# Performance work log

Measured on AMD Instinct MI355X. Metric: run time of the kernel, lower is better.

The kernel has to match this reference:

```python
import jax, jax.numpy as jnp
import numpy as np

B, H, W, C = 4, 16, 16, 1024
D_INNER, D_STATE, DT_RANK, K = 2048, 32, 64, 4
NTXT = 4096
L = H * W


def _selective_scan(u, dt, A, Bs, Cs, Ds):
    # u, dt: (B,K,D,L); A: (K,D,N); Bs, Cs: (B,K,N,L); Ds: (K,D)
    u_l = jnp.moveaxis(u, -1, 0)
    dt_l = jnp.moveaxis(dt, -1, 0)
    B_l = jnp.moveaxis(Bs, -1, 0)
    C_l = jnp.moveaxis(Cs, -1, 0)
    h0 = jnp.zeros(u.shape[:3] + (A.shape[-1],), u.dtype)

    def step(h, xs):
        u_t, dt_t, B_t, C_t = xs
        dA = jnp.exp(dt_t[..., None] * A)                    # (B,K,D,N)
        h = h * dA + dt_t[..., None] * B_t[:, :, None, :] * u_t[..., None]
        y = jnp.einsum('bkdn,bkn->bkd', h, C_t)
        return h, y

    _, ys = jax.lax.scan(step, h0, (u_l, dt_l, B_l, C_l))
    return jnp.moveaxis(ys, 0, -1) + Ds[None, :, :, None] * u


def _forward(image_embeds, text_embeds, in_proj_w, conv_w, conv_b, x_proj_w,
             dt_proj_w, dt_proj_b, A_logs, Ds, out_norm_w, out_norm_b, out_proj_w):
    b = image_embeds.shape[0]
    # in_proj -> split into x (scanned) and z (gate)
    xz = jnp.einsum('bhwc,ec->bhwe', image_embeds, in_proj_w)    # (B,H,W,2*D_INNER)
    x, z = jnp.split(xz, 2, axis=-1)
    # depthwise conv 3x3 + SiLU
    xc = jnp.transpose(x, (0, 3, 1, 2))                          # (B,D,H,W)
    xc = jax.lax.conv_general_dilated(xc, conv_w, (1, 1), 'SAME',
                                      feature_group_count=D_INNER,
                                      dimension_numbers=('NCHW', 'OIHW', 'NCHW'))
    xc = jax.nn.silu(xc + conv_b[None, :, None, None])
    # cross-scan: row-major, col-major, and their reverses
    xm = xc.reshape(b, D_INNER, L)
    xt = jnp.transpose(xc, (0, 1, 3, 2)).reshape(b, D_INNER, L)
    xs = jnp.stack([xm, xt, xm[..., ::-1], xt[..., ::-1]], axis=1)  # (B,4,D,L)
    # low-rank input-dependent params
    x_dbl = jnp.einsum('bkdl,kcd->bkcl', xs, x_proj_w)
    dts, Bmat, Cmat = jnp.split(x_dbl, [DT_RANK, DT_RANK + D_STATE], axis=2)
    dts = jnp.einsum('bkrl,kdr->bkdl', dts, dt_proj_w)
    dts = jax.nn.softplus(dts + dt_proj_b[None, :, :, None])
    A = -jnp.exp(A_logs).reshape(K, D_INNER, D_STATE)
    ys = _selective_scan(xs, dts, A, Bmat, Cmat, Ds.reshape(K, D_INNER))
    # cross-merge
    y = ys[:, 0] + ys[:, 2, :, ::-1]
    y_col = ys[:, 1] + ys[:, 3, :, ::-1]
    y = y + jnp.transpose(y_col.reshape(b, D_INNER, W, H), (0, 1, 3, 2)).reshape(b, D_INNER, L)
    # out_norm (LayerNorm over channels) + gate + out_proj
    y = jnp.transpose(y, (0, 2, 1))                              # (B,L,D)
    mu = y.mean(-1, keepdims=True)
    var = ((y - mu) ** 2).mean(-1, keepdims=True)
    y = (y - mu) * jax.lax.rsqrt(var + 1e-5) * out_norm_w + out_norm_b
    y = y.reshape(b, H, W, D_INNER) * jax.nn.silu(z)
    enhanced = jnp.einsum('bhwd,cd->bhwc', y, out_proj_w)        # (B,H,W,C)
    # L2 normalize + similarity logits
    img = enhanced / jnp.linalg.norm(enhanced, axis=-1, keepdims=True)
    txt = text_embeds / jnp.linalg.norm(text_embeds, axis=-1, keepdims=True)
    return jnp.matmul(img, txt.T)                                # (B,H,W,NTXT)


def setup_inputs() -> dict:
    key = jax.random.key(0)
    ks = jax.random.split(key, 8)
    s = 0.02
    return dict(
        image_embeds=jax.random.normal(ks[0], (B, H, W, C), jnp.float32),
        text_embeds=jax.random.normal(ks[1], (NTXT, C), jnp.float32),
        in_proj_w=jax.random.normal(ks[2], (2 * D_INNER, C), jnp.float32) * s,
        conv_w=jax.random.normal(ks[3], (D_INNER, 1, 3, 3), jnp.float32) * s,
        conv_b=jnp.zeros((D_INNER,), jnp.float32),
        x_proj_w=jax.random.normal(ks[4], (K, DT_RANK + 2 * D_STATE, D_INNER), jnp.float32) * s,
        dt_proj_w=jax.random.normal(ks[5], (K, D_INNER, DT_RANK), jnp.float32) * s,
        dt_proj_b=jax.random.normal(ks[6], (K, D_INNER), jnp.float32) * s,
        A_logs=jnp.log(jnp.broadcast_to(jnp.arange(1, D_STATE + 1, dtype=jnp.float32), (K * D_INNER, D_STATE)).copy()),
        Ds=jnp.ones((K * D_INNER,), jnp.float32),
        out_norm_w=jnp.ones((D_INNER,), jnp.float32),
        out_norm_b=jnp.zeros((D_INNER,), jnp.float32),
        out_proj_w=jax.random.normal(ks[7], (C, D_INNER), jnp.float32) * s,
    )


def reference(image_embeds, text_embeds, in_proj_w, conv_w, conv_b, x_proj_w,
              dt_proj_w, dt_proj_b, A_logs, Ds, out_norm_w, out_norm_b, out_proj_w):
    return _forward(image_embeds, text_embeds, in_proj_w, conv_w, conv_b, x_proj_w,
                    dt_proj_w, dt_proj_b, A_logs, Ds, out_norm_w, out_norm_b, out_proj_w)
```

## Files before the change

### kernel.cpp

```cpp
#include <hip/hip_runtime.h>
#include <math.h>


typedef unsigned short u16;
typedef __attribute__((ext_vector_type(8))) short short8;
typedef __attribute__((ext_vector_type(8))) unsigned short ushort8;
typedef __attribute__((ext_vector_type(4))) float f32x4;

__device__ __forceinline__ float sigmoidf_(float x) { return 1.f / (1.f + __expf(-x)); }

__device__ __forceinline__ u16 f2bf(float x) {
  unsigned u = __float_as_uint(x);
  unsigned r = u + 0x7FFFu + ((u >> 16) & 1u);
  return (u16)(r >> 16);
}
__device__ __forceinline__ float bf2f(u16 h) { return __uint_as_float((unsigned)h << 16); }

__device__ __forceinline__ void gl_lds16(const u16* g, u16* l) {
  __builtin_amdgcn_global_load_lds((__attribute__((address_space(1))) void*)g,
                                   (__attribute__((address_space(3))) void*)l, 16, 0, 0);
}

__global__ __launch_bounds__(256) void cvt_swz(
    const float* __restrict__ in, u16* __restrict__ hi, u16* __restrict__ lo,
    int R, int bpr , int lda)
{
  long t = (long)blockIdx.x * 256 + threadIdx.x;
  if (t >= (long)R * bpr) return;
  int m = (int)(t / bpr);
  int rb = (int)(t - (long)m * bpr);
  int kc = rb >> 2, g = rb & 3;
  const float* src = in + (long)m * lda + (kc << 5) + (g << 2);
  float4 a = *(const float4*)src;
  float4 b = *(const float4*)(src + 16);
  float v[8] = {a.x, a.y, a.z, a.w, b.x, b.y, b.z, b.w};
  ushort8 H, L;
#pragma unroll
  for (int q = 0; q < 8; q++) {
    u16 h = f2bf(v[q]);
    H[q] = h;
    L[q] = f2bf(v[q] - bf2f(h));
  }
  long off = (((long)kc * R + m) << 5) + ((long)((g ^ ((m >> 1) & 3)) << 3));
  *(ushort8*)(hi + off) = H;
  *(ushort8*)(lo + off) = L;
}

__global__ __launch_bounds__(256) void mfma_nt(
    const u16* __restrict__ Ahi, const u16* __restrict__ Alo,
    const u16* __restrict__ Bhi, const u16* __restrict__ Blo,
    float* __restrict__ C, int Mtot, int Ntot, int Ksteps, int ldc,
    int sArows, int sBrows, int bmod, long sC, long sCk, int ksplit)
{
  __shared__ u16 smem[16384];
  const int tid = threadIdx.x, lane = tid & 63, wid = tid >> 6;
  const int zb = blockIdx.z / ksplit, zk = blockIdx.z - zb * ksplit;
  const int m0 = blockIdx.y << 7, n0 = blockIdx.x << 7;

  const u16* sg;
  long row0;
  int tot;
  if (wid < 2) { row0 = (long)zb * sArows + m0; tot = Mtot; sg = wid ? Alo : Ahi; }
  else         { row0 = (long)(zb % bmod) * sBrows + n0; tot = Ntot; sg = (wid == 3) ? Blo : Bhi; }
  u16* sl = smem + (wid << 12);
  const int laneoff = lane << 3;

  f32x4 acc[4][4];
#pragma unroll
  for (int i = 0; i < 4; i++)
#pragma unroll
    for (int j = 0; j < 4; j++) acc[i][j] = (f32x4)0.f;

  const int wr = wid >> 1, wc = wid & 1;
  const int fr = lane & 15, g = lane >> 4;
  int offA[4], offB[4];
#pragma unroll
  for (int i = 0; i < 4; i++) {
    int rA = wr * 64 + i * 16 + fr;
    offA[i] = rA * 32 + ((g ^ ((rA >> 1) & 3)) << 3);
    int rB = wc * 64 + i * 16 + fr;
    offB[i] = rB * 32 + ((g ^ ((rB >> 1) & 3)) << 3);
  }

  for (int kc = 0; kc < Ksteps; ++kc) {
    const int kcg = zk * Ksteps + kc;
    const u16* s = sg + ((long)kcg * tot + row0) * 32 + laneoff;
#pragma unroll
    for (int c = 0; c < 8; ++c) gl_lds16(s + c * 512, sl + c * 512 + laneoff);
    asm volatile("s_waitcnt vmcnt(0)" ::: "memory");
    __syncthreads();

    short8 ah[4], al[4], bh[4], bl[4];
#pragma unroll
    for (int i = 0; i < 4; i++) {
      ah[i] = *(const short8*)(smem + offA[i]);
      al[i] = *(const short8*)(smem + 4096 + offA[i]);
      bh[i] = *(const short8*)(smem + 8192 + offB[i]);
      bl[i] = *(const short8*)(smem + 12288 + offB[i]);
    }
#pragma unroll
    for (int i = 0; i < 4; i++)
#pragma unroll
      for (int j = 0; j < 4; j++) {
        acc[i][j] = __builtin_amdgcn_mfma_f32_16x16x32_bf16(ah[i], bh[j], acc[i][j], 0, 0, 0);
        acc[i][j] = __builtin_amdgcn_mfma_f32_16x16x32_bf16(ah[i], bl[j], acc[i][j], 0, 0, 0);
        acc[i][j] = __builtin_amdgcn_mfma_f32_16x16x32_bf16(al[i], bh[j], acc[i][j], 0, 0, 0);
      }
    __syncthreads();
  }

  float* Cb = C + (long)zb * sC + (long)zk * sCk;
  const int r0 = m0 + wr * 64, c0 = n0 + wc * 64;
#pragma unroll
  for (int i = 0; i < 4; i++)
#pragma unroll
    for (int j = 0; j < 4; j++) {
      const long cc = c0 + j * 16 + fr;
#pragma unroll
      for (int q = 0; q < 4; q++)
        Cb[(long)(r0 + i * 16 + g * 4 + q) * ldc + cc] = acc[i][j][q];
    }
}

__global__ __launch_bounds__(256) void sum8(float* __restrict__ px)
{
  long t = (long)blockIdx.x * 256 + threadIdx.x;
  if (t >= 524288) return;
  float s = px[t];
#pragma unroll
  for (int p = 1; p < 8; p++) s += px[(long)p * 524288 + t];
  px[t] = s;
}

__global__ __launch_bounds__(256) void zero_buf(float4* __restrict__ p)
{
  p[(long)blockIdx.x * 256 + threadIdx.x] = (float4){0.f, 0.f, 0.f, 0.f};
}

__global__ __launch_bounds__(256) void conv_scatter_bf16(
    const float* __restrict__ xz, const float* __restrict__ cw,
    const float* __restrict__ cb, u16* __restrict__ hi, u16* __restrict__ lo)
{
  const int p = blockIdx.x & 255;
  const int b = blockIdx.x >> 8;
  const int h = p >> 4, w = p & 15;
  const int l1 = (w << 4) + h;
  const int pos[4] = {p, l1, 255 - p, 255 - l1};
#pragma unroll
  for (int it = 0; it < 8; it++) {
    const int d = it * 256 + threadIdx.x;
    float acc = cb[d];
#pragma unroll
    for (int dh = 0; dh < 3; dh++) {
      const int hh = h + dh - 1;
      if (hh < 0 || hh > 15) continue;
#pragma unroll
      for (int dw = 0; dw < 3; dw++) {
        const int ww = w + dw - 1;
        if (ww < 0 || ww > 15) continue;
        acc = fmaf(xz[((long)(b * 256 + (hh << 4) + ww)) * 4096 + d],
                   cw[d * 9 + dh * 3 + dw], acc);
      }
    }
    const float sv = acc * sigmoidf_(acc);
    const u16 hv = f2bf(sv);
    const u16 lv = f2bf(sv - bf2f(hv));
    const int kc = d >> 5, dd = d & 31;
    const int g0 = (dd < 16) ? (dd >> 2) : ((dd - 16) >> 2);
    const int slot = (dd < 16) ? (dd & 3) : 4 + ((dd - 16) & 3);
#pragma unroll
    for (int kk = 0; kk < 4; kk++) {
      const int m = (b * 4 + kk) * 256 + pos[kk];
      const long off = (((long)kc * 4096 + m) << 5) + ((g0 ^ ((m >> 1) & 3)) << 3) + slot;
      hi[off] = hv;
      lo[off] = lv;
    }
  }
}

__global__ __launch_bounds__(256) void scan_fused(
    const u16* __restrict__ xs_hi, const u16* __restrict__ xs_lo,
    const float* __restrict__ xdbl, const float* __restrict__ w_dt,
    const float* __restrict__ b_dt, const float* __restrict__ A_logs,
    const float* __restrict__ Dsv, float* __restrict__ ym)
{
  const int tid = threadIdx.x;
  const int sub = tid & 1;
  const int dl = tid >> 1;
  const int d = blockIdx.x * 128 + dl;
  const int k = blockIdx.y, b = blockIdx.z;
  const int bk = b * 4 + k;
  const int kd = k * 2048 + d;
  const int n0 = sub * 16;

  float a[16], hst[16];
#pragma unroll
  for (int j = 0; j < 16; j++) {
    a[j] = -__expf(A_logs[(long)kd * 32 + n0 + j]);
    hst[j] = 0.f;
  }
  const float Dval = Dsv[kd];
  const float bias = b_dt[kd];

  float wdt[32];
  const float* wp = w_dt + (long)kd * 64 + sub * 32;
#pragma unroll
  for (int j = 0; j < 32; j += 4) *(float4*)&wdt[j] = *(const float4*)(wp + j);

  const int dd = d & 31;
  const int g0 = (dd < 16) ? (dd >> 2) : ((dd - 16) >> 2);
  const int slot = (dd < 16) ? (dd & 3) : 4 + ((dd - 16) & 3);
  const int kcl = dl >> 5;

  const float* xb = xdbl + (long)bk * 256 * 128;
  const int mbase = bk * 256;
  const long obase = (long)b * 256 * 2048 + d;

  __shared__ float xd[32][128];
  __shared__ u16 uh[4][32][32];
  __shared__ u16 ul[4][32][32];

  for (int l0 = 0; l0 < 256; l0 += 32) {
    __syncthreads();
#pragma unroll
    for (int i = 0; i < 4; i++) {
      const int idx = i * 256 + tid;
      const int r = idx >> 5, c = idx & 31;
      *(float4*)&xd[r][c * 4] = *(const float4*)(xb + (l0 + r) * 128 + c * 4);
    }
#pragma unroll
    for (int i = 0; i < 2; i++) {
      const int j = i * 256 + tid;
      const int kc2 = j >> 7, r = (j >> 2) & 31, part = j & 3;
      const long go = (((long)(blockIdx.x * 4 + kc2) * 4096 + mbase + l0 + r) << 5) + part * 8;
      *(ushort8*)&uh[kc2][r][part * 8] = *(const ushort8*)(xs_hi + go);
      *(ushort8*)&ul[kc2][r][part * 8] = *(const ushort8*)(xs_lo + go);
    }
    __syncthreads();

    for (int ls = 0; ls < 32; ls++) {
      const int l = l0 + ls;
      const int m = mbase + l;
      float da = 0.f;
#pragma unroll
      for (int r4 = 0; r4 < 8; r4++) {
        const float4 xv = *(const float4*)&xd[ls][sub * 32 + r4 * 4];
        da = fmaf(wdt[r4 * 4 + 0], xv.x, da);
        da = fmaf(wdt[r4 * 4 + 1], xv.y, da);
        da = fmaf(wdt[r4 * 4 + 2], xv.z, da);
        da = fmaf(wdt[r4 * 4 + 3], xv.w, da);
      }
      da += __shfl_xor(da, 1);
      const float xsp = da + bias;
      const float dt = (xsp > 20.f) ? xsp : log1pf(__expf(xsp));
      const int sw = ((g0 ^ ((m >> 1) & 3)) << 3) + slot;
      const float u = bf2f(uh[kcl][ls][sw]) + bf2f(ul[kcl][ls][sw]);
      const float dtu = dt * u;
      float y = 0.f;
#pragma unroll
      for (int j = 0; j < 16; j++) {
        const float dA = __expf(a[j] * dt);
        hst[j] = fmaf(hst[j], dA, dtu * xd[ls][64 + n0 + j]);
        y = fmaf(hst[j], xd[ls][96 + n0 + j], y);
      }
      y += __shfl_xor(y, 1);
      if (sub == 0) {
        int p;
        if (k == 0) p = l;
        else if (k == 1) p = ((l & 15) << 4) + (l >> 4);
        else if (k == 2) p = 255 - l;
        else { const int lr = 255 - l; p = ((lr & 15) << 4) + (lr >> 4); }
        atomicAdd(&ym[obase + (long)p * 2048], fmaf(Dval, u, y));
      }
    }
  }
}

__global__ __launch_bounds__(256) void ln_gate_cvt(
    const float* __restrict__ ym, const float* __restrict__ xz,
    const float* __restrict__ lw, const float* __restrict__ lb,
    u16* __restrict__ hi, u16* __restrict__ lo)
{
  const int row = blockIdx.x;
  const int tid = threadIdx.x;
  const float* yr = ym + (long)row * 2048;

  __shared__ float sg[2048];
  __shared__ float sm[8];
  float v[8];
  float s = 0.f, ss = 0.f;
#pragma unroll
  for (int i = 0; i < 8; i++) {
    const float t = yr[i * 256 + tid];
    v[i] = t;
    s += t;
    ss += t * t;
  }
#pragma unroll
  for (int off = 32; off > 0; off >>= 1) {
    s += __shfl_down(s, off);
    ss += __shfl_down(ss, off);
  }
  const int lane = tid & 63, wid = tid >> 6;
  if (lane == 0) { sm[wid] = s; sm[4 + wid] = ss; }
  __syncthreads();
  const float S = sm[0] + sm[1] + sm[2] + sm[3];
  const float SS = sm[4] + sm[5] + sm[6] + sm[7];
  const float mu = S * (1.f / 2048.f);
  const float var = SS * (1.f / 2048.f) - mu * mu;
  const float inv = rsqrtf(var + 1e-5f);
#pragma unroll
  for (int i = 0; i < 8; i++) {
    const int d = i * 256 + tid;
    const float yn = (v[i] - mu) * inv * lw[d] + lb[d];
    const float zz = xz[(long)row * 4096 + 2048 + d];
    sg[d] = yn * zz * sigmoidf_(zz);
  }
  __syncthreads();
  const int kc = tid >> 2, g = tid & 3;
  const int c0 = kc * 32 + g * 4;
  ushort8 H, L;
#pragma unroll
  for (int q = 0; q < 4; q++) {
    const float f0 = sg[c0 + q], f1 = sg[c0 + 16 + q];
    const u16 h0 = f2bf(f0), h1 = f2bf(f1);
    H[q] = h0; H[4 + q] = h1;
    L[q] = f2bf(f0 - bf2f(h0));
    L[4 + q] = f2bf(f1 - bf2f(h1));
  }
  const long off = (((long)kc * 1024 + row) << 5) + ((long)((g ^ ((row >> 1) & 3)) << 3));
  *(ushort8*)(hi + off) = H;
  *(ushort8*)(lo + off) = L;
}

template <int P>
__global__ __launch_bounds__(256) void l2cvt(
    const float* __restrict__ in, long pstride,
    u16* __restrict__ hi, u16* __restrict__ lo, int R)
{
  const int row = blockIdx.x;
  const int tid = threadIdx.x;
  __shared__ float sg[1024];
  __shared__ float sm[4];
  float ss = 0.f;
  for (int i = tid; i < 1024; i += 256) {
    float v = in[(long)row * 1024 + i];
#pragma unroll
    for (int p2 = 1; p2 < P; p2++) v += in[(long)p2 * pstride + (long)row * 1024 + i];
    sg[i] = v;
    ss += v * v;
  }
#pragma unroll
  for (int off = 32; off > 0; off >>= 1) ss += __shfl_down(ss, off);
  const int lane = tid & 63, wid = tid >> 6;
  if (lane == 0) sm[wid] = ss;
  __syncthreads();
  const float sc = rsqrtf(sm[0] + sm[1] + sm[2] + sm[3]);
  if (tid < 128) {
    const int kc = tid >> 2, g = tid & 3;
    const int c0 = kc * 32 + g * 4;
    ushort8 H, L;
#pragma unroll
    for (int q = 0; q < 4; q++) {
      const float f0 = sg[c0 + q] * sc, f1 = sg[c0 + 16 + q] * sc;
      const u16 h0 = f2bf(f0), h1 = f2bf(f1);
      H[q] = h0; H[4 + q] = h1;
      L[q] = f2bf(f0 - bf2f(h0));
      L[4 + q] = f2bf(f1 - bf2f(h1));
    }
    const long off = (((long)kc * R + row) << 5) + ((long)((g ^ ((row >> 1) & 3)) << 3));
    *(ushort8*)(hi + off) = H;
    *(ushort8*)(lo + off) = L;
  }
}

extern "C" void kernel_launch(void* const* d_in, const int* in_sizes, int n_in,
                              void* d_out, int out_size, void* d_ws, size_t ws_size,
                              hipStream_t stream)
{
  const float* img = (const float*)d_in[0];
  const float* txt = (const float*)d_in[1];
  const float* w_in = (const float*)d_in[2];
  const float* conv_w = (const float*)d_in[3];
  const float* conv_b = (const float*)d_in[4];
  const float* w_x = (const float*)d_in[5];
  const float* w_dt = (const float*)d_in[6];
  const float* b_dt = (const float*)d_in[7];
  const float* A_logs = (const float*)d_in[8];
  const float* Dsv = (const float*)d_in[9];
  const float* ln_w = (const float*)d_in[10];
  const float* ln_b = (const float*)d_in[11];
  const float* w_out = (const float*)d_in[12];
  float* out = (float*)d_out;

  float* ws = (float*)d_ws;
  float* xz = ws;
  float* Cr = ws + 4194304;
  u16* imgsw_h = (u16*)Cr;
  u16* imgsw_l = (u16*)(Cr + 524288);
  u16* w_insw_h = (u16*)(Cr + 1048576);
  u16* w_insw_l = (u16*)(Cr + 3145728);
  u16* xs_hi = (u16*)Cr;
  u16* xs_lo = (u16*)(Cr + 4194304);
  u16* outgsw_h = (u16*)Cr;
  u16* outgsw_l = (u16*)(Cr + 1048576);
  u16* w_outsw_h = (u16*)(Cr + 2097152);
  u16* w_outsw_l = (u16*)(Cr + 3145728);
  u16* enhsw_h = (u16*)(Cr + 4194304);
  u16* enhsw_l = (u16*)(Cr + 4718592);
  u16* w_xsw_h = (u16*)(ws + 12582912);
  u16* w_xsw_l = (u16*)(ws + 13107200);
  float* ym = ws + 13631488;
  u16* txtnsw_h = (u16*)xz;
  u16* txtnsw_l = (u16*)(xz + 2097152);

  float* ob = (float*)d_out;
  float* px8 = ob;
  float* xdbl = px8;
  float* px4 = ob;

  cvt_swz<<<512, 256, 0, stream>>>(img, imgsw_h, imgsw_l, 1024, 128, 1024);
  cvt_swz<<<2048, 256, 0, stream>>>(w_in, w_insw_h, w_insw_l, 4096, 128, 1024);
  cvt_swz<<<512, 256, 0, stream>>>(w_x, w_xsw_h, w_xsw_l, 512, 256, 2048);

  mfma_nt<<<dim3(32, 8, 1), 256, 0, stream>>>(imgsw_h, imgsw_l, w_insw_h, w_insw_l,
                                              xz, 1024, 4096, 32, 4096, 0, 0, 1, 0, 0, 1);

  conv_scatter_bf16<<<dim3(1024), 256, 0, stream>>>(xz, conv_w, conv_b, xs_hi, xs_lo);

  mfma_nt<<<dim3(1, 2, 128), 256, 0, stream>>>(xs_hi, xs_lo, w_xsw_h, w_xsw_l,
                                               px8, 4096, 512, 8, 128, 256, 128, 4,
                                               32768, 524288, 8);
  sum8<<<2048, 256, 0, stream>>>(px8);
  zero_buf<<<2048, 256, 0, stream>>>((float4*)ym);

  scan_fused<<<dim3(16, 4, 4), 256, 0, stream>>>(xs_hi, xs_lo, xdbl, w_dt, b_dt,
                                                 A_logs, Dsv, ym);

  ln_gate_cvt<<<dim3(1024), 256, 0, stream>>>(ym, xz, ln_w, ln_b, outgsw_h, outgsw_l);

  cvt_swz<<<1024, 256, 0, stream>>>(w_out, w_outsw_h, w_outsw_l, 1024, 256, 2048);

  mfma_nt<<<dim3(8, 8, 4), 256, 0, stream>>>(outgsw_h, outgsw_l, w_outsw_h, w_outsw_l,
                                             px4, 1024, 1024, 16, 1024, 0, 0, 1,
                                             0, 1048576, 4);

  l2cvt<4><<<dim3(1024), 256, 0, stream>>>(px4, 1048576, enhsw_h, enhsw_l, 1024);
  l2cvt<1><<<dim3(4096), 256, 0, stream>>>(txt, 0, txtnsw_h, txtnsw_l, 4096);

  mfma_nt<<<dim3(32, 8, 1), 256, 0, stream>>>(enhsw_h, enhsw_l, txtnsw_h, txtnsw_l,
                                              out, 1024, 4096, 32, 4096, 0, 0, 1, 0, 0, 1);
}
```

Before: 523.7 us.

## Split scan state across 4 lanes and precompute dt per chunk in shared memory

```diff
diff --git a/kernel.cpp b/kernel.cpp
--- a/kernel.cpp
+++ b/kernel.cpp
@@ -185,40 +185,39 @@
     const float* __restrict__ Dsv, float* __restrict__ ym)
 {
   const int tid = threadIdx.x;
-  const int sub = tid & 1;
-  const int dl = tid >> 1;
-  const int d = blockIdx.x * 128 + dl;
   const int k = blockIdx.y, b = blockIdx.z;
   const int bk = b * 4 + k;
+  const int dbase = blockIdx.x << 6;
+  const int mbase = bk * 256;
+  const int kc0 = dbase >> 5;
+
+  const int dc = tid >> 2, sub = tid & 3;
+  const int d = dbase + dc;
   const int kd = k * 2048 + d;
-  const int n0 = sub * 16;
-
-  float a[16], hst[16];
-#pragma unroll
-  for (int j = 0; j < 16; j++) {
+  const int n0 = sub * 8;
+
+  float a[8], hst[8];
+#pragma unroll
+  for (int j = 0; j < 8; j++) {
     a[j] = -__expf(A_logs[(long)kd * 32 + n0 + j]);
     hst[j] = 0.f;
   }
   const float Dval = Dsv[kd];
-  const float bias = b_dt[kd];
-
-  float wdt[32];
-  const float* wp = w_dt + (long)kd * 64 + sub * 32;
-#pragma unroll
-  for (int j = 0; j < 32; j += 4) *(float4*)&wdt[j] = *(const float4*)(wp + j);
-
-  const int dd = d & 31;
-  const int g0 = (dd < 16) ? (dd >> 2) : ((dd - 16) >> 2);
-  const int slot = (dd < 16) ? (dd & 3) : 4 + ((dd - 16) & 3);
-  const int kcl = dl >> 5;
+  const long obase = (long)b * 256 * 2048 + d;
+
+  const int lam = tid & 63, wv = tid >> 6;
+  const int kdd = k * 2048 + dbase + lam;
+  float wdt[64];
+  const float* wp = w_dt + (long)kdd * 64;
+#pragma unroll
+  for (int c = 0; c < 64; c += 4) *(float4*)&wdt[c] = *(const float4*)(wp + c);
+  const float bdt = b_dt[kdd];
 
   const float* xb = xdbl + (long)bk * 256 * 128;
-  const int mbase = bk * 256;
-  const long obase = (long)b * 256 * 2048 + d;
 
   __shared__ float xd[32][128];
-  __shared__ u16 uh[4][32][32];
-  __shared__ u16 ul[4][32][32];
+  __shared__ float dtS[32][64];
+  __shared__ float uS[32][64];
 
   for (int l0 = 0; l0 < 256; l0 += 32) {
     __syncthreads();
@@ -228,42 +227,54 @@
       const int r = idx >> 5, c = idx & 31;
       *(float4*)&xd[r][c * 4] = *(const float4*)(xb + (l0 + r) * 128 + c * 4);
     }
-#pragma unroll
-    for (int i = 0; i < 2; i++) {
-      const int j = i * 256 + tid;
-      const int kc2 = j >> 7, r = (j >> 2) & 31, part = j & 3;
-      const long go = (((long)(blockIdx.x * 4 + kc2) * 4096 + mbase + l0 + r) << 5) + part * 8;
-      *(ushort8*)&uh[kc2][r][part * 8] = *(const ushort8*)(xs_hi + go);
-      *(ushort8*)&ul[kc2][r][part * 8] = *(const ushort8*)(xs_lo + go);
+    {
+      const int r = tid >> 3, kcl = (tid >> 2) & 1, part = tid & 3;
+      const int m = mbase + l0 + r;
+      const long go = (((long)(kc0 + kcl) * 4096 + m) << 5) + part * 8;
+      const ushort8 Hv = *(const ushort8*)(xs_hi + go);
+      const ushort8 Lv = *(const ushort8*)(xs_lo + go);
+      const int gx = part ^ ((m >> 1) & 3);
+      float lo4[4], hi4[4];
+#pragma unroll
+      for (int q = 0; q < 4; q++) {
+        lo4[q] = bf2f(Hv[q]) + bf2f(Lv[q]);
+        hi4[q] = bf2f(Hv[4 + q]) + bf2f(Lv[4 + q]);
+      }
+      *(float4*)&uS[r][kcl * 32 + gx * 4] = *(float4*)lo4;
+      *(float4*)&uS[r][kcl * 32 + 16 + gx * 4] = *(float4*)hi4;
     }
     __syncthreads();
-
+#pragma unroll
+    for (int s = 0; s < 8; s++) {
+      const int ls = wv * 8 + s;
+      float acc = 0.f;
+#pragma unroll
+      for (int c4 = 0; c4 < 16; c4++) {
+        const float4 xv = *(const float4*)&xd[ls][c4 * 4];
+        acc = fmaf(wdt[c4 * 4 + 0], xv.x, acc);
+        acc = fmaf(wdt[c4 * 4 + 1], xv.y, acc);
+        acc = fmaf(wdt[c4 * 4 + 2], xv.z, acc);
+        acc = fmaf(wdt[c4 * 4 + 3], xv.w, acc);
+      }
+      const float xsp = acc + bdt;
+      dtS[ls][lam] = (xsp > 20.f) ? xsp : log1pf(__expf(xsp));
+    }
+    __syncthreads();
+#pragma unroll 4
     for (int ls = 0; ls < 32; ls++) {
       const int l = l0 + ls;
-      const int m = mbase + l;
-      float da = 0.f;
-#pragma unroll
-      for (int r4 = 0; r4 < 8; r4++) {
-        const float4 xv = *(const float4*)&xd[ls][sub * 32 + r4 * 4];
-        da = fmaf(wdt[r4 * 4 + 0], xv.x, da);
-        da = fmaf(wdt[r4 * 4 + 1], xv.y, da);
-        da = fmaf(wdt[r4 * 4 + 2], xv.z, da);
-        da = fmaf(wdt[r4 * 4 + 3], xv.w, da);
-      }
-      da += __shfl_xor(da, 1);
-      const float xsp = da + bias;
-      const float dt = (xsp > 20.f) ? xsp : log1pf(__expf(xsp));
-      const int sw = ((g0 ^ ((m >> 1) & 3)) << 3) + slot;
-      const float u = bf2f(uh[kcl][ls][sw]) + bf2f(ul[kcl][ls][sw]);
+      const float dt = dtS[ls][dc];
+      const float u = uS[ls][dc];
       const float dtu = dt * u;
       float y = 0.f;
 #pragma unroll
-      for (int j = 0; j < 16; j++) {
+      for (int j = 0; j < 8; j++) {
         const float dA = __expf(a[j] * dt);
         hst[j] = fmaf(hst[j], dA, dtu * xd[ls][64 + n0 + j]);
         y = fmaf(hst[j], xd[ls][96 + n0 + j], y);
       }
       y += __shfl_xor(y, 1);
+      y += __shfl_xor(y, 2);
       if (sub == 0) {
         int p;
         if (k == 0) p = l;
@@ -434,7 +445,7 @@
   sum8<<<2048, 256, 0, stream>>>(px8);
   zero_buf<<<2048, 256, 0, stream>>>((float4*)ym);
 
-  scan_fused<<<dim3(16, 4, 4), 256, 0, stream>>>(xs_hi, xs_lo, xdbl, w_dt, b_dt,
+  scan_fused<<<dim3(32, 4, 4), 256, 0, stream>>>(xs_hi, xs_lo, xdbl, w_dt, b_dt,
                                                  A_logs, Dsv, ym);
 
   ln_gate_cvt<<<dim3(1024), 256, 0, stream>>>(ym, xz, ln_w, ln_b, outgsw_h, outgsw_l);
```

Measured after the change: 434.4 us. -17.1%, faster.
